# Kernel tuning notes

Hardware: AMD Instinct MI355X
Metric: run time of the kernel (lower is better)

Reference implementation:

```python
import jax, jax.numpy as jnp
import numpy as np

NUM_DOCS = 1_000_000
VOCAB = 30522
NNZ_PER_ROW = 64
NNZ = NUM_DOCS * NNZ_PER_ROW
Q_NNZ = 32
SHARDS = 4
TOP_K = 100


def setup_inputs() -> dict:
    key = jax.random.key(0)
    k1, k2, k3, k4 = jax.random.split(key, 4)
    doc_values = jax.random.uniform(k1, (NNZ,), dtype=jnp.float32)          # CSR values (impact weights)
    doc_indices = jax.random.randint(k2, (NNZ,), 0, VOCAB, dtype=jnp.int32)  # CSR column indices
    row_ids = (jnp.arange(NNZ, dtype=jnp.int32) // NNZ_PER_ROW)              # expanded crow -> sorted row ids
    q_indices = jax.random.randint(k3, (Q_NNZ,), 0, VOCAB, dtype=jnp.int32)
    q_values = jax.random.uniform(k4, (Q_NNZ,), dtype=jnp.float32)
    return {
        "doc_values": doc_values,
        "q_values": q_values,
        "doc_indices": doc_indices,
        "row_ids": row_ids,
        "q_indices": q_indices,
    }


def reference(doc_values, q_values, doc_indices, row_ids, q_indices):
    # build_dense_query: sparse COO -> dense (duplicates coalesced by summation)
    query = jnp.zeros((VOCAB,), dtype=doc_values.dtype).at[q_indices].add(q_values)
    # CSR SpMV: per-nnz contribution gathered from query, summed per row
    contrib = doc_values * query[doc_indices]                                 # [NNZ]
    scores = jax.ops.segment_sum(contrib, row_ids, num_segments=NUM_DOCS,
                                 indices_are_sorted=True)                     # [NUM_DOCS]
    # per-shard top-k (equal row split, matching _split_csr)
    rows_per_shard = NUM_DOCS // SHARDS
    shard_scores = scores.reshape(SHARDS, rows_per_shard)
    loc_s, loc_i = jax.lax.top_k(shard_scores, TOP_K)                         # [SHARDS, K]
    offsets = (jnp.arange(SHARDS, dtype=loc_i.dtype) * rows_per_shard)[:, None]
    all_scores = loc_s.reshape(-1)                                            # [SHARDS*K]
    all_indices = (loc_i + offsets).reshape(-1)
    # merge_topk_results: global top-k over concatenated shard candidates
    top_scores, sel = jax.lax.top_k(all_scores, TOP_K)
    top_indices = all_indices[sel]
    return top_scores, top_indices
```

## Files before the change

### kernel.cpp

```cpp
#include <hip/hip_runtime.h>

#define NUM_DOCS 1000000
#define VOCAB 30522
#define NNZ 64000000LL
#define Q_NNZ 32
#define TOP_K 100
#define CAND_MAX 4096
#define BM_WORDS 954

#define OFF_Q       0
#define OFF_HIST    30528
#define OFF_COUNTER (OFF_HIST + 65536)
#define OFF_THRESH  (OFF_COUNTER + 1)
#define OFF_CANDS   (OFF_COUNTER + 16)
#define OFF_CANDI   (OFF_CANDS + CAND_MAX)
#define OFF_SCORES  (OFF_CANDI + CAND_MAX)
#define ZERO_WORDS  (OFF_COUNTER + 16)

__global__ void scatter_q_kernel(const float* __restrict__ qv, const int* __restrict__ qi,
                                 float* __restrict__ q) {
    int i = threadIdx.x;
    if (i < Q_NNZ) atomicAdd(&q[qi[i]], qv[i]);
}

__global__ void score_kernel(const float* __restrict__ dv, const int* __restrict__ di,
                             const int* __restrict__ qi, const float* __restrict__ qg,
                             float* __restrict__ scores) {
    __shared__ unsigned bm[BM_WORDS];
    for (int i = threadIdx.x; i < BM_WORDS; i += blockDim.x) bm[i] = 0u;
    __syncthreads();
    if (threadIdx.x < Q_NNZ) {
        int v = qi[threadIdx.x];
        atomicOr(&bm[v >> 5], 1u << (v & 31));
    }
    __syncthreads();

    long long t = (long long)blockIdx.x * blockDim.x + threadIdx.x;
    long long base = t * 16;
    const float4* dv4 = (const float4*)(dv + base);
    const int4*   di4 = (const int4*)(di + base);
    float sum = 0.f;
#pragma unroll
    for (int j = 0; j < 4; ++j) {
        float4 v = dv4[j];
        int4   x = di4[j];
        if ((bm[x.x >> 5] >> (x.x & 31)) & 1u) sum += v.x * qg[x.x];
        if ((bm[x.y >> 5] >> (x.y & 31)) & 1u) sum += v.y * qg[x.y];
        if ((bm[x.z >> 5] >> (x.z & 31)) & 1u) sum += v.z * qg[x.z];
        if ((bm[x.w >> 5] >> (x.w & 31)) & 1u) sum += v.w * qg[x.w];
    }
    sum += __shfl_xor(sum, 1);
    sum += __shfl_xor(sum, 2);
    if ((t & 3) == 0) scores[t >> 2] = sum;
}

__global__ void hist_kernel(const float* __restrict__ scores, unsigned* __restrict__ hist) {
    int i = blockIdx.x * blockDim.x + threadIdx.x;
    if (i < NUM_DOCS) {
        float s = scores[i];
        if (s > 0.f) atomicAdd(&hist[__float_as_uint(s) >> 16], 1u);
    }
}

__global__ void thresh_kernel(const unsigned* __restrict__ hist, unsigned* __restrict__ thresh) {
    __shared__ unsigned part[256];
    int t = threadIdx.x;
    unsigned s = 0;
    const unsigned* h = hist + t * 256;
    for (int j = 0; j < 256; ++j) s += h[j];
    part[t] = s;
    __syncthreads();
    if (t == 0) {
        unsigned cum = 0;
        int c = 255;
        for (; c >= 0; --c) {
            if (cum + part[c] >= TOP_K) break;
            cum += part[c];
        }
        unsigned bin = 1;
        if (c >= 0) {
            int b = c * 256 + 255;
            for (; b >= c * 256; --b) {
                cum += hist[b];
                if (cum >= TOP_K) break;
            }
            if (b < c * 256) b = c * 256;
            bin = (unsigned)b;
        }
        thresh[0] = bin << 16;
    }
}

__global__ void gather_kernel(const float* __restrict__ scores, const unsigned* __restrict__ thresh,
                              unsigned* __restrict__ counter,
                              float* __restrict__ cs, int* __restrict__ ci) {
    int i = blockIdx.x * blockDim.x + threadIdx.x;
    if (i < NUM_DOCS) {
        float s = scores[i];
        if (__float_as_uint(s) >= thresh[0]) {
            unsigned p = atomicAdd(counter, 1u);
            if (p < CAND_MAX) { cs[p] = s; ci[p] = i; }
        }
    }
}

__global__ void topk_kernel(const unsigned* __restrict__ counter,
                            const float* __restrict__ cs, const int* __restrict__ ci,
                            float* __restrict__ out) {
    __shared__ float ls[CAND_MAX];
    __shared__ int   li[CAND_MAX];
    int n = (int)min(counter[0], (unsigned)CAND_MAX);
    for (int i = threadIdx.x; i < n; i += 64) { ls[i] = cs[i]; li[i] = ci[i]; }
    __syncthreads();
    for (int k = 0; k < TOP_K; ++k) {
        float best = -1.f; int bestd = 0x7fffffff; int bestp = -1;
        for (int i = threadIdx.x; i < n; i += 64) {
            float s = ls[i];
            int   d = li[i];
            if (s > best || (s == best && d < bestd)) { best = s; bestd = d; bestp = i; }
        }
        for (int off = 1; off < 64; off <<= 1) {
            float os = __shfl_xor(best,  off);
            int   od = __shfl_xor(bestd, off);
            int   op = __shfl_xor(bestp, off);
            if (os > best || (os == best && od < bestd)) { best = os; bestd = od; bestp = op; }
        }
        if (threadIdx.x == 0) {
            out[k]         = (bestp >= 0) ? best : 0.f;
            out[TOP_K + k] = (float)((bestp >= 0) ? bestd : 0);
            if (bestp >= 0) ls[bestp] = -1.f;
        }
        __syncthreads();
    }
}

extern "C" void kernel_launch(void* const* d_in, const int* in_sizes, int n_in,
                              void* d_out, int out_size, void* d_ws, size_t ws_size,
                              hipStream_t stream) {
    const float* doc_values  = (const float*)d_in[0];
    const float* q_values    = (const float*)d_in[1];
    const int*   doc_indices = (const int*)d_in[2];
    const int*   q_indices   = (const int*)d_in[4];
    float* out = (float*)d_out;

    float*    ws      = (float*)d_ws;
    float*    q       = ws + OFF_Q;
    unsigned* hist    = (unsigned*)d_ws + OFF_HIST;
    unsigned* counter = (unsigned*)d_ws + OFF_COUNTER;
    unsigned* thresh  = (unsigned*)d_ws + OFF_THRESH;
    float*    cs      = ws + OFF_CANDS;
    int*      ci      = (int*)d_ws + OFF_CANDI;
    float*    scores  = ws + OFF_SCORES;

    hipMemsetAsync(d_ws, 0, (size_t)ZERO_WORDS * 4, stream);

    scatter_q_kernel<<<1, 64, 0, stream>>>(q_values, q_indices, q);

    score_kernel<<<15625, 256, 0, stream>>>(doc_values, doc_indices, q_indices, q, scores);

    int blocks1m = (NUM_DOCS + 255) / 256;
    hist_kernel<<<blocks1m, 256, 0, stream>>>(scores, hist);
    thresh_kernel<<<1, 256, 0, stream>>>(hist, thresh);
    gather_kernel<<<blocks1m, 256, 0, stream>>>(scores, thresh, counter, cs, ci);
    topk_kernel<<<1, 64, 0, stream>>>(counter, cs, ci, out);
}
```

Measured before the change: 751.9 us.

## Fuse histogram into score kernel, remap to 16 threads per doc, parallelize threshold

```diff
diff --git a/kernel.cpp b/kernel.cpp
--- a/kernel.cpp
+++ b/kernel.cpp
@@ -10,12 +10,15 @@
 
 #define OFF_Q       0
 #define OFF_HIST    30528
-#define OFF_COUNTER (OFF_HIST + 65536)
+#define OFF_PART    (OFF_HIST + 65536)
+#define OFF_DONE    (OFF_PART + 256)
+#define OFF_COUNTER (OFF_DONE + 1)
 #define OFF_THRESH  (OFF_COUNTER + 1)
-#define OFF_CANDS   (OFF_COUNTER + 16)
+#define OFF_CTRLEND (OFF_THRESH + 13)
+#define OFF_CANDS   OFF_CTRLEND
 #define OFF_CANDI   (OFF_CANDS + CAND_MAX)
 #define OFF_SCORES  (OFF_CANDI + CAND_MAX)
-#define ZERO_WORDS  (OFF_COUNTER + 16)
+#define ZERO_WORDS  OFF_CTRLEND
 
 __global__ void scatter_q_kernel(const float* __restrict__ qv, const int* __restrict__ qi,
                                  float* __restrict__ q) {
@@ -23,11 +26,12 @@
     if (i < Q_NNZ) atomicAdd(&q[qi[i]], qv[i]);
 }
 
-__global__ void score_kernel(const float* __restrict__ dv, const int* __restrict__ di,
-                             const int* __restrict__ qi, const float* __restrict__ qg,
-                             float* __restrict__ scores) {
+__global__ __launch_bounds__(256) void score_kernel(
+        const float* __restrict__ dv, const int* __restrict__ di,
+        const int* __restrict__ qi, const float* __restrict__ qg,
+        float* __restrict__ scores, unsigned* __restrict__ hist) {
     __shared__ unsigned bm[BM_WORDS];
-    for (int i = threadIdx.x; i < BM_WORDS; i += blockDim.x) bm[i] = 0u;
+    for (int i = threadIdx.x; i < BM_WORDS; i += 256) bm[i] = 0u;
     __syncthreads();
     if (threadIdx.x < Q_NNZ) {
         int v = qi[threadIdx.x];
@@ -35,57 +39,74 @@
     }
     __syncthreads();
 
-    long long t = (long long)blockIdx.x * blockDim.x + threadIdx.x;
-    long long base = t * 16;
-    const float4* dv4 = (const float4*)(dv + base);
-    const int4*   di4 = (const int4*)(di + base);
-    float sum = 0.f;
-#pragma unroll
-    for (int j = 0; j < 4; ++j) {
-        float4 v = dv4[j];
-        int4   x = di4[j];
-        if ((bm[x.x >> 5] >> (x.x & 31)) & 1u) sum += v.x * qg[x.x];
-        if ((bm[x.y >> 5] >> (x.y & 31)) & 1u) sum += v.y * qg[x.y];
-        if ((bm[x.z >> 5] >> (x.z & 31)) & 1u) sum += v.z * qg[x.z];
-        if ((bm[x.w >> 5] >> (x.w & 31)) & 1u) sum += v.w * qg[x.w];
-    }
-    sum += __shfl_xor(sum, 1);
-    sum += __shfl_xor(sum, 2);
-    if ((t & 3) == 0) scores[t >> 2] = sum;
-}
-
-__global__ void hist_kernel(const float* __restrict__ scores, unsigned* __restrict__ hist) {
-    int i = blockIdx.x * blockDim.x + threadIdx.x;
-    if (i < NUM_DOCS) {
-        float s = scores[i];
+    int t = blockIdx.x * 256 + threadIdx.x;
+    long long base = (long long)t * 4;
+    int4 x = *(const int4*)(di + base);
+    float s = 0.f;
+    if ((bm[x.x >> 5] >> (x.x & 31)) & 1u) s += dv[base + 0] * qg[x.x];
+    if ((bm[x.y >> 5] >> (x.y & 31)) & 1u) s += dv[base + 1] * qg[x.y];
+    if ((bm[x.z >> 5] >> (x.z & 31)) & 1u) s += dv[base + 2] * qg[x.z];
+    if ((bm[x.w >> 5] >> (x.w & 31)) & 1u) s += dv[base + 3] * qg[x.w];
+    s += __shfl_xor(s, 1);
+    s += __shfl_xor(s, 2);
+    s += __shfl_xor(s, 4);
+    s += __shfl_xor(s, 8);
+    if ((threadIdx.x & 15) == 0) {
+        int doc = t >> 4;
+        scores[doc] = s;
         if (s > 0.f) atomicAdd(&hist[__float_as_uint(s) >> 16], 1u);
     }
 }
 
-__global__ void thresh_kernel(const unsigned* __restrict__ hist, unsigned* __restrict__ thresh) {
-    __shared__ unsigned part[256];
-    int t = threadIdx.x;
-    unsigned s = 0;
-    const unsigned* h = hist + t * 256;
-    for (int j = 0; j < 256; ++j) s += h[j];
-    part[t] = s;
+__global__ __launch_bounds__(256) void thresh_kernel(
+        const unsigned* __restrict__ hist, unsigned* __restrict__ part,
+        unsigned* __restrict__ done, unsigned* __restrict__ thresh) {
+    int b = blockIdx.x, t = threadIdx.x;
+    unsigned v = hist[b * 256 + t];
+    unsigned s = v;
+    for (int off = 1; off < 64; off <<= 1) s += __shfl_xor(s, off);
+    __shared__ unsigned wsum[4];
+    if ((t & 63) == 0) wsum[t >> 6] = s;
     __syncthreads();
+    if (t == 0) {
+        atomicAdd(&part[b], wsum[0] + wsum[1] + wsum[2] + wsum[3]);
+        __threadfence();
+    }
+    __shared__ int lastflag;
+    if (t == 0) lastflag = (atomicAdd(done, 1u) == 255u) ? 1 : 0;
+    __syncthreads();
+    if (!lastflag) return;
+
+    __shared__ unsigned parts[256];
+    parts[t] = atomicAdd(&part[t], 0u);
+    __syncthreads();
+    __shared__ int sc;
+    __shared__ unsigned scum;
     if (t == 0) {
         unsigned cum = 0;
         int c = 255;
         for (; c >= 0; --c) {
-            if (cum + part[c] >= TOP_K) break;
-            cum += part[c];
+            if (cum + parts[c] >= TOP_K) break;
+            cum += parts[c];
         }
+        sc = c; scum = cum;
+    }
+    __syncthreads();
+    int c = sc;
+    __shared__ unsigned bins[256];
+    if (c >= 0) bins[t] = hist[c * 256 + t];
+    __syncthreads();
+    if (t == 0) {
         unsigned bin = 1;
         if (c >= 0) {
-            int b = c * 256 + 255;
-            for (; b >= c * 256; --b) {
-                cum += hist[b];
+            unsigned cum = scum;
+            int b2 = 255;
+            for (; b2 >= 0; --b2) {
+                cum += bins[b2];
                 if (cum >= TOP_K) break;
             }
-            if (b < c * 256) b = c * 256;
-            bin = (unsigned)b;
+            if (b2 < 0) b2 = 0;
+            bin = (unsigned)(c * 256 + b2);
         }
         thresh[0] = bin << 16;
     }
@@ -146,6 +167,8 @@
     float*    ws      = (float*)d_ws;
     float*    q       = ws + OFF_Q;
     unsigned* hist    = (unsigned*)d_ws + OFF_HIST;
+    unsigned* part    = (unsigned*)d_ws + OFF_PART;
+    unsigned* done    = (unsigned*)d_ws + OFF_DONE;
     unsigned* counter = (unsigned*)d_ws + OFF_COUNTER;
     unsigned* thresh  = (unsigned*)d_ws + OFF_THRESH;
     float*    cs      = ws + OFF_CANDS;
@@ -156,11 +179,11 @@
 
     scatter_q_kernel<<<1, 64, 0, stream>>>(q_values, q_indices, q);
 
-    score_kernel<<<15625, 256, 0, stream>>>(doc_values, doc_indices, q_indices, q, scores);
+    score_kernel<<<62500, 256, 0, stream>>>(doc_values, doc_indices, q_indices, q, scores, hist);
+
+    thresh_kernel<<<256, 256, 0, stream>>>(hist, part, done, thresh);
 
     int blocks1m = (NUM_DOCS + 255) / 256;
-    hist_kernel<<<blocks1m, 256, 0, stream>>>(scores, hist);
-    thresh_kernel<<<1, 256, 0, stream>>>(hist, thresh);
     gather_kernel<<<blocks1m, 256, 0, stream>>>(scores, thresh, counter, cs, ci);
     topk_kernel<<<1, 64, 0, stream>>>(counter, cs, ci, out);
 }
```

Result: faster. 649.0 us (-13.7%).
